# Kernel optimization log

Hardware: AMD Instinct MI355X
Metric: run time of the kernel (lower is better)

Reference implementation:

```python
import jax, jax.numpy as jnp
import numpy as np

BN_EPS = 1e-5


def setup_inputs() -> dict:
    key = jax.random.key(0)
    ks = jax.random.split(key, 12)
    N, E, H, INV = 100000, 500000, 128, 16
    DIN = 2 * H + INV  # 272
    x_send = jax.random.normal(ks[0], (N, H), dtype=jnp.float32)
    x_rec = jax.random.normal(ks[1], (N, H), dtype=jnp.float32)
    index = jax.random.randint(ks[2], (2, E), 0, N, dtype=jnp.int64)
    edge_attr = jax.random.normal(ks[3], (E, INV), dtype=jnp.float32)
    # message_mlp = BatchNorm1d(272) -> Linear(272,128) -> SiLU  (eval-mode BN)
    bn_gamma = jax.random.normal(ks[4], (DIN,), dtype=jnp.float32) * 0.1 + 1.0
    bn_beta = jax.random.normal(ks[5], (DIN,), dtype=jnp.float32) * 0.1
    bn_mean = jax.random.normal(ks[6], (DIN,), dtype=jnp.float32) * 0.1
    bn_var = jax.random.uniform(ks[7], (DIN,), dtype=jnp.float32) + 0.5
    W1 = jax.random.normal(ks[8], (DIN, H), dtype=jnp.float32) / np.sqrt(DIN)
    b1 = jnp.zeros((H,), dtype=jnp.float32)
    # edge_inf_mlp = Linear(128,1) -> Sigmoid
    W2 = jax.random.normal(ks[9], (H, 1), dtype=jnp.float32) / np.sqrt(H)
    b2 = jnp.zeros((1,), dtype=jnp.float32)
    return {"x_send": x_send, "x_rec": x_rec, "index": index, "edge_attr": edge_attr,
            "bn_gamma": bn_gamma, "bn_beta": bn_beta, "bn_mean": bn_mean, "bn_var": bn_var,
            "W1": W1, "b1": b1, "W2": W2, "b2": b2}


def reference(x_send, x_rec, index, edge_attr, bn_gamma, bn_beta, bn_mean, bn_var, W1, b1, W2, b2):
    idx_send, idx_rec = index[0], index[1]
    # gather + concat -> [E, 2H + INV]
    state = jnp.concatenate((x_send[idx_send], x_rec[idx_rec], edge_attr), axis=1)
    # eval-mode BatchNorm1d
    state = (state - bn_mean) * (bn_gamma * jax.lax.rsqrt(bn_var + BN_EPS)) + bn_beta
    # Linear + SiLU
    messages = jax.nn.silu(state @ W1 + b1)  # [E, H]
    # edge gating: Linear(H,1) + Sigmoid
    edge_weights = jax.nn.sigmoid(messages @ W2 + b2)  # [E, 1]
    # scatter_add aggregation over receiving nodes
    return jax.ops.segment_sum(messages * edge_weights, idx_rec, num_segments=x_rec.shape[0])
```

## Files before the change

kernel.cpp:

```cpp
#include <hip/hip_runtime.h>
#include <hip/hip_bf16.h>
#include <hip/hip_fp16.h>
#include <math.h>

#define HDIM 128
#define INVD 16
#define DIN 272
#define NKT 9

typedef __attribute__((ext_vector_type(4))) float f32x4;
typedef __attribute__((ext_vector_type(8))) short bf16x8;
typedef __attribute__((ext_vector_type(2))) __fp16 fp16x2;

__device__ inline short f2bf(float f) {
    union { float f; unsigned u; } v; v.f = f;
    unsigned r = v.u + 0x7FFFu + ((v.u >> 16) & 1u);
    return (short)(r >> 16);
}

template<bool WS>
__global__ __launch_bounds__(256, 2) void etnn_kernel(
    const float* __restrict__ x_send,
    const float* __restrict__ x_rec,
    const int*   __restrict__ index,
    const float* __restrict__ edge_attr,
    const float* __restrict__ bn_gamma,
    const float* __restrict__ bn_beta,
    const float* __restrict__ bn_mean,
    const float* __restrict__ bn_var,
    const float* __restrict__ W1,
    const float* __restrict__ b1,
    const float* __restrict__ W2,
    const float* __restrict__ b2,
    float* __restrict__ out,
    __half* __restrict__ ws,
    int E, int nIter)
{
    __shared__ short btab[NKT * 8 * 64 * 8];
    __shared__ float scl[DIN];
    __shared__ float shf[DIN];
    __shared__ float bias2[2][HDIM];
    __shared__ float biasT[HDIM];

    const int tid = threadIdx.x;
    const int l  = tid & 63;
    const int lr = l & 15;
    const int lg = l >> 4;

    for (int c = tid; c < DIN; c += 256) {
        float sc = bn_gamma[c] * rsqrtf(bn_var[c] + 1e-5f);
        scl[c] = sc;
        shf[c] = bn_beta[c] - bn_mean[c] * sc;
    }
    __syncthreads();

    for (int f = tid; f < NKT * 8 * 64; f += 256) {
        const int kk  = f >> 9;
        const int cb  = (f >> 6) & 7;
        const int ln  = f & 63;
        const int k0  = kk * 32 + (ln >> 4) * 8;
        const int col = cb * 16 + (ln & 15);
        bf16x8 bv;
        #pragma unroll
        for (int j = 0; j < 8; ++j) {
            const int k = k0 + j;
            float v = (k < DIN) ? scl[k] * W1[k * HDIM + col] : 0.f;
            bv[j] = f2bf(v);
        }
        *(bf16x8*)&btab[f * 8] = bv;
    }
    {
        const int col  = tid & 127;
        const int half = tid >> 7;
        float s = 0.f;
        for (int k = half * 136; k < half * 136 + 136; ++k)
            s += shf[k] * W1[k * HDIM + col];
        bias2[half][col] = s;
    }
    __syncthreads();
    if (tid < HDIM) biasT[tid] = b1[tid] + bias2[0][tid] + bias2[1][tid];
    __syncthreads();

    float biasv[8], w2v[8];
    #pragma unroll
    for (int cb = 0; cb < 8; ++cb) {
        biasv[cb] = biasT[cb * 16 + lr];
        w2v[cb]   = W2[cb * 16 + lr];
    }
    const float b2v = b2[0];
    const bool evn = !(lr & 1);

    const int gw = blockIdx.x * 4 + (tid >> 6);
    const int NW = gridDim.x * 4;

    for (int it = gw; it < nIter; it += NW) {
        const int e0 = it * 16;
        const int e  = e0 + lr;
        const int ec = (e < E) ? e : E - 1;
        const int is = index[ec];
        const int ir = index[E + ec];

        const f32x4* ps = (const f32x4*)(x_send + (size_t)is * HDIM);
        const f32x4* pr = (const f32x4*)(x_rec  + (size_t)ir * HDIM);
        f32x4 Ls[8], Lr[8], La[2];
        #pragma unroll
        for (int kk = 0; kk < 4; ++kk) {
            Ls[kk * 2]     = ps[kk * 8 + lg * 2];
            Ls[kk * 2 + 1] = ps[kk * 8 + lg * 2 + 1];
            Lr[kk * 2]     = pr[kk * 8 + lg * 2];
            Lr[kk * 2 + 1] = pr[kk * 8 + lg * 2 + 1];
        }
        if (lg < 2) {
            const f32x4* pa = (const f32x4*)(edge_attr + (size_t)ec * INVD + lg * 8);
            La[0] = pa[0]; La[1] = pa[1];
        } else {
            La[0] = (f32x4){0.f, 0.f, 0.f, 0.f};
            La[1] = (f32x4){0.f, 0.f, 0.f, 0.f};
        }

        f32x4 acc[8];
        #pragma unroll
        for (int cb = 0; cb < 8; ++cb) acc[cb] = (f32x4){0.f, 0.f, 0.f, 0.f};

        #pragma unroll
        for (int kk = 0; kk < NKT; ++kk) {
            f32x4 lo = (kk < 4) ? Ls[kk * 2]     : (kk < 8) ? Lr[(kk - 4) * 2]     : La[0];
            f32x4 hi = (kk < 4) ? Ls[kk * 2 + 1] : (kk < 8) ? Lr[(kk - 4) * 2 + 1] : La[1];
            bf16x8 a;
            a[0] = f2bf(lo[0]); a[1] = f2bf(lo[1]); a[2] = f2bf(lo[2]); a[3] = f2bf(lo[3]);
            a[4] = f2bf(hi[0]); a[5] = f2bf(hi[1]); a[6] = f2bf(hi[2]); a[7] = f2bf(hi[3]);
            #pragma unroll
            for (int cb = 0; cb < 8; ++cb) {
                bf16x8 b = *(const bf16x8*)&btab[((kk * 8 + cb) * 64 + l) * 8];
                acc[cb] = __builtin_amdgcn_mfma_f32_16x16x32_bf16(a, b, acc[cb], 0, 0, 0);
            }
        }

        float p[4] = {0.f, 0.f, 0.f, 0.f};
        #pragma unroll
        for (int cb = 0; cb < 8; ++cb) {
            #pragma unroll
            for (int q = 0; q < 4; ++q) {
                float z = acc[cb][q] + biasv[cb];
                float m = z / (1.f + __expf(-z));
                acc[cb][q] = m;
                p[q] += m * w2v[cb];
            }
        }
        #pragma unroll
        for (int q = 0; q < 4; ++q) {
            p[q] += __shfl_xor(p[q], 1, 64);
            p[q] += __shfl_xor(p[q], 2, 64);
            p[q] += __shfl_xor(p[q], 4, 64);
            p[q] += __shfl_xor(p[q], 8, 64);
        }

        #pragma unroll
        for (int q = 0; q < 4; ++q) {
            const int row = lg * 4 + q;
            if (e0 + row < E) {
                const int irq = __shfl(ir, row, 64);
                const float g = 1.f / (1.f + __expf(-(p[q] + b2v)));
                if constexpr (WS) {
                    float m[8];
                    #pragma unroll
                    for (int cb = 0; cb < 8; ++cb) m[cb] = acc[cb][q] * g;
                    #pragma unroll
                    for (int c = 0; c < 4; ++c) {
                        float x0 = __shfl_xor(m[2 * c],     1, 64);
                        float x1 = __shfl_xor(m[2 * c + 1], 1, 64);
                        float va = evn ? m[2 * c] : x1;
                        float vb = evn ? x0       : m[2 * c + 1];
                        union { fp16x2 h; unsigned u; } pk;
                        pk.h = __builtin_amdgcn_cvt_pkrtz(va, vb);
                        const int col0 = evn ? (32 * c + lr) : (32 * c + 15 + lr);
                        unsigned long long a =
                            (unsigned long long)(ws + (size_t)irq * HDIM + col0);
                        asm volatile("global_atomic_pk_add_f16 %0, %1, off"
                                     :: "v"(a), "v"(pk.u) : "memory");
                    }
                } else {
                    float* orow = out + (size_t)irq * HDIM + lr;
                    #pragma unroll
                    for (int cb = 0; cb < 8; ++cb)
                        atomicAdd(orow + cb * 16, acc[cb][q] * g);
                }
            }
        }
    }
}

__global__ __launch_bounds__(256) void cvt_kernel(const __half* __restrict__ ws,
                                                  float* __restrict__ out, int n) {
    int i = (blockIdx.x * 256 + threadIdx.x) * 4;
    if (i < n) {
        const __half2* p = (const __half2*)(ws + i);
        float2 a = __half22float2(p[0]);
        float2 b = __half22float2(p[1]);
        f32x4 v = {a.x, a.y, b.x, b.y};
        *(f32x4*)(out + i) = v;
    }
}

extern "C" void kernel_launch(void* const* d_in, const int* in_sizes, int n_in,
                              void* d_out, int out_size, void* d_ws, size_t ws_size,
                              hipStream_t stream) {
    const float* x_send    = (const float*)d_in[0];
    const float* x_rec     = (const float*)d_in[1];
    const int*   index     = (const int*)d_in[2];
    const float* edge_attr = (const float*)d_in[3];
    const float* bn_gamma  = (const float*)d_in[4];
    const float* bn_beta   = (const float*)d_in[5];
    const float* bn_mean   = (const float*)d_in[6];
    const float* bn_var    = (const float*)d_in[7];
    const float* W1        = (const float*)d_in[8];
    const float* b1        = (const float*)d_in[9];
    const float* W2        = (const float*)d_in[10];
    const float* b2        = (const float*)d_in[11];
    float* out = (float*)d_out;

    const int E = in_sizes[3] / INVD;
    const int N = in_sizes[0] / HDIM;
    const int nIter = (E + 15) / 16;
    const int grid = 512;

    const size_t need = (size_t)N * HDIM * sizeof(__half);
    if (ws_size >= need) {
        __half* ws = (__half*)d_ws;
        hipMemsetAsync(ws, 0, need, stream);
        etnn_kernel<true><<<grid, 256, 0, stream>>>(x_send, x_rec, index, edge_attr,
                                                    bn_gamma, bn_beta, bn_mean, bn_var,
                                                    W1, b1, W2, b2, out, ws, E, nIter);
        const int n = N * HDIM;
        cvt_kernel<<<(n / 4 + 255) / 256, 256, 0, stream>>>(ws, out, n);
    } else {
        hipMemsetAsync(d_out, 0, (size_t)out_size * sizeof(float), stream);
        etnn_kernel<false><<<grid, 256, 0, stream>>>(x_send, x_rec, index, edge_attr,
                                                     bn_gamma, bn_beta, bn_mean, bn_var,
                                                     W1, b1, W2, b2, out, nullptr, E, nIter);
    }
}
```

Baseline: 193.7 us.

## Sort edges by receiver via counting sort and merge same-node atomics

Adds histogram, single-block scan and fill kernels that build a receiver-sorted edge permutation in the workspace. The main kernel then processes edges in that order and accumulates consecutive messages for the same receiver in registers, issuing fp16 atomics only when the node changes. The aim is fewer scattered atomic operations and better locality for x_rec gathers. In exchange it adds three extra launches, a serial-ish single-block scan over 100k nodes, an extra indirection load, and lanes in a 4-row group rarely share a receiver (average degree about 5), so the merging gains may be small.

```diff
diff --git a/kernel.cpp b/kernel.cpp
--- a/kernel.cpp
+++ b/kernel.cpp
@@ -18,7 +18,42 @@
     return (short)(r >> 16);
 }
 
-template<bool WS>
+__global__ void hist_kernel(const int* __restrict__ index, int* __restrict__ cnt, int E) {
+    int e = blockIdx.x * blockDim.x + threadIdx.x;
+    if (e < E) atomicAdd(&cnt[index[E + e]], 1);
+}
+
+__global__ __launch_bounds__(1024) void scan_kernel(const int* __restrict__ cnt,
+                                                    int* __restrict__ cur, int N) {
+    __shared__ int psum[1024];
+    const int t = threadIdx.x;
+    const int C = (N + 1023) >> 10;
+    const int a0 = t * C;
+    const int a1 = (a0 + C < N) ? a0 + C : N;
+    int s = 0;
+    for (int i = a0; i < a1; ++i) s += cnt[i];
+    psum[t] = s;
+    __syncthreads();
+    for (int d = 1; d < 1024; d <<= 1) {
+        int v = (t >= d) ? psum[t - d] : 0;
+        __syncthreads();
+        psum[t] += v;
+        __syncthreads();
+    }
+    int run = (t > 0) ? psum[t - 1] : 0;
+    for (int i = a0; i < a1; ++i) {
+        cur[i] = run;
+        run += cnt[i];
+    }
+}
+
+__global__ void fill_kernel(const int* __restrict__ index, int* __restrict__ cur,
+                            int* __restrict__ eid, int E) {
+    int e = blockIdx.x * blockDim.x + threadIdx.x;
+    if (e < E) { int p = atomicAdd(&cur[index[E + e]], 1); eid[p] = e; }
+}
+
+template<int MODE>
 __global__ __launch_bounds__(256, 2) void etnn_kernel(
     const float* __restrict__ x_send,
     const float* __restrict__ x_rec,
@@ -32,6 +67,7 @@
     const float* __restrict__ b1,
     const float* __restrict__ W2,
     const float* __restrict__ b2,
+    const int*   __restrict__ eid,
     float* __restrict__ out,
     __half* __restrict__ ws,
     int E, int nIter)
@@ -95,8 +131,9 @@
 
     for (int it = gw; it < nIter; it += NW) {
         const int e0 = it * 16;
-        const int e  = e0 + lr;
-        const int ec = (e < E) ? e : E - 1;
+        const int pos = e0 + lr;
+        const int pc  = (pos < E) ? pos : E - 1;
+        const int ec  = (MODE == 2) ? eid[pc] : pc;
         const int is = index[ec];
         const int ir = index[E + ec];
 
@@ -155,35 +192,74 @@
             p[q] += __shfl_xor(p[q], 8, 64);
         }
 
-        #pragma unroll
-        for (int q = 0; q < 4; ++q) {
-            const int row = lg * 4 + q;
-            if (e0 + row < E) {
-                const int irq = __shfl(ir, row, 64);
-                const float g = 1.f / (1.f + __expf(-(p[q] + b2v)));
-                if constexpr (WS) {
-                    float m[8];
-                    #pragma unroll
-                    for (int cb = 0; cb < 8; ++cb) m[cb] = acc[cb][q] * g;
-                    #pragma unroll
-                    for (int c = 0; c < 4; ++c) {
-                        float x0 = __shfl_xor(m[2 * c],     1, 64);
-                        float x1 = __shfl_xor(m[2 * c + 1], 1, 64);
-                        float va = evn ? m[2 * c] : x1;
-                        float vb = evn ? x0       : m[2 * c + 1];
-                        union { fp16x2 h; unsigned u; } pk;
-                        pk.h = __builtin_amdgcn_cvt_pkrtz(va, vb);
-                        const int col0 = evn ? (32 * c + lr) : (32 * c + 15 + lr);
-                        unsigned long long a =
-                            (unsigned long long)(ws + (size_t)irq * HDIM + col0);
-                        asm volatile("global_atomic_pk_add_f16 %0, %1, off"
-                                     :: "v"(a), "v"(pk.u) : "memory");
+        if constexpr (MODE == 2) {
+            float mm[8];
+            int cur = -1;
+            auto flushf = [&](int node) {
+                #pragma unroll
+                for (int c = 0; c < 4; ++c) {
+                    float x0 = __shfl_xor(mm[2 * c],     1, 64);
+                    float x1 = __shfl_xor(mm[2 * c + 1], 1, 64);
+                    float va = evn ? mm[2 * c] : x1;
+                    float vb = evn ? x0        : mm[2 * c + 1];
+                    union { fp16x2 h; unsigned u; } pk;
+                    pk.h = __builtin_amdgcn_cvt_pkrtz(va, vb);
+                    const int col0 = evn ? (32 * c + lr) : (32 * c + 15 + lr);
+                    unsigned long long a =
+                        (unsigned long long)(ws + (size_t)node * HDIM + col0);
+                    asm volatile("global_atomic_pk_add_f16 %0, %1, off"
+                                 :: "v"(a), "v"(pk.u) : "memory");
+                }
+            };
+            #pragma unroll
+            for (int q = 0; q < 4; ++q) {
+                const int row = lg * 4 + q;
+                if (e0 + row < E) {
+                    const int nq = __shfl(ir, row, 64);
+                    const float g = 1.f / (1.f + __expf(-(p[q] + b2v)));
+                    if (nq != cur) {
+                        if (cur >= 0) flushf(cur);
+                        cur = nq;
+                        #pragma unroll
+                        for (int cb = 0; cb < 8; ++cb) mm[cb] = acc[cb][q] * g;
+                    } else {
+                        #pragma unroll
+                        for (int cb = 0; cb < 8; ++cb) mm[cb] += acc[cb][q] * g;
                     }
-                } else {
-                    float* orow = out + (size_t)irq * HDIM + lr;
-                    #pragma unroll
-                    for (int cb = 0; cb < 8; ++cb)
-                        atomicAdd(orow + cb * 16, acc[cb][q] * g);
+                }
+            }
+            if (cur >= 0) flushf(cur);
+        } else {
+            #pragma unroll
+            for (int q = 0; q < 4; ++q) {
+                const int row = lg * 4 + q;
+                if (e0 + row < E) {
+                    const int irq = __shfl(ir, row, 64);
+                    const float g = 1.f / (1.f + __expf(-(p[q] + b2v)));
+                    if constexpr (MODE == 1) {
+                        float m[8];
+                        #pragma unroll
+                        for (int cb = 0; cb < 8; ++cb) m[cb] = acc[cb][q] * g;
+                        #pragma unroll
+                        for (int c = 0; c < 4; ++c) {
+                            float x0 = __shfl_xor(m[2 * c],     1, 64);
+                            float x1 = __shfl_xor(m[2 * c + 1], 1, 64);
+                            float va = evn ? m[2 * c] : x1;
+                            float vb = evn ? x0       : m[2 * c + 1];
+                            union { fp16x2 h; unsigned u; } pk;
+                            pk.h = __builtin_amdgcn_cvt_pkrtz(va, vb);
+                            const int col0 = evn ? (32 * c + lr) : (32 * c + 15 + lr);
+                            unsigned long long a =
+                                (unsigned long long)(ws + (size_t)irq * HDIM + col0);
+                            asm volatile("global_atomic_pk_add_f16 %0, %1, off"
+                                         :: "v"(a), "v"(pk.u) : "memory");
+                        }
+                    } else {
+                        float* orow = out + (size_t)irq * HDIM + lr;
+                        #pragma unroll
+                        for (int cb = 0; cb < 8; ++cb)
+                            atomicAdd(orow + cb * 16, acc[cb][q] * g);
+                    }
                 }
             }
         }
@@ -224,19 +300,37 @@
     const int nIter = (E + 15) / 16;
     const int grid = 512;
 
-    const size_t need = (size_t)N * HDIM * sizeof(__half);
-    if (ws_size >= need) {
+    const size_t accBytes = (size_t)N * HDIM * sizeof(__half);
+    const size_t accAl    = (accBytes + 255) & ~(size_t)255;
+    const size_t csrBytes = ((size_t)2 * N + (size_t)E) * sizeof(int);
+
+    if (ws_size >= accAl + csrBytes) {
         __half* ws = (__half*)d_ws;
-        hipMemsetAsync(ws, 0, need, stream);
-        etnn_kernel<true><<<grid, 256, 0, stream>>>(x_send, x_rec, index, edge_attr,
-                                                    bn_gamma, bn_beta, bn_mean, bn_var,
-                                                    W1, b1, W2, b2, out, ws, E, nIter);
+        int* cnt = (int*)((char*)d_ws + accAl);
+        int* cur = cnt + N;
+        int* eid = cur + N;
+        hipMemsetAsync(ws, 0, accBytes, stream);
+        hipMemsetAsync(cnt, 0, (size_t)N * sizeof(int), stream);
+        hist_kernel<<<(E + 255) / 256, 256, 0, stream>>>(index, cnt, E);
+        scan_kernel<<<1, 1024, 0, stream>>>(cnt, cur, N);
+        fill_kernel<<<(E + 255) / 256, 256, 0, stream>>>(index, cur, eid, E);
+        etnn_kernel<2><<<grid, 256, 0, stream>>>(x_send, x_rec, index, edge_attr,
+                                                 bn_gamma, bn_beta, bn_mean, bn_var,
+                                                 W1, b1, W2, b2, eid, out, ws, E, nIter);
+        const int n = N * HDIM;
+        cvt_kernel<<<(n / 4 + 255) / 256, 256, 0, stream>>>(ws, out, n);
+    } else if (ws_size >= accBytes) {
+        __half* ws = (__half*)d_ws;
+        hipMemsetAsync(ws, 0, accBytes, stream);
+        etnn_kernel<1><<<grid, 256, 0, stream>>>(x_send, x_rec, index, edge_attr,
+                                                 bn_gamma, bn_beta, bn_mean, bn_var,
+                                                 W1, b1, W2, b2, nullptr, out, ws, E, nIter);
         const int n = N * HDIM;
         cvt_kernel<<<(n / 4 + 255) / 256, 256, 0, stream>>>(ws, out, n);
     } else {
         hipMemsetAsync(d_out, 0, (size_t)out_size * sizeof(float), stream);
-        etnn_kernel<false><<<grid, 256, 0, stream>>>(x_send, x_rec, index, edge_attr,
-                                                     bn_gamma, bn_beta, bn_mean, bn_var,
-                                                     W1, b1, W2, b2, out, nullptr, E, nIter);
-    }
-}
+        etnn_kernel<0><<<grid, 256, 0, stream>>>(x_send, x_rec, index, edge_attr,
+                                                 bn_gamma, bn_beta, bn_mean, bn_var,
+                                                 W1, b1, W2, b2, nullptr, out, nullptr, E, nIter);
+    }
+}
```

New measurement: 380.6 us. 1.97x slower.

## Process two edge tiles per iteration and use packed bf16 conversion

Applied to the files above, without the earlier changes.

Each wave now loads indices and issues the row gathers for two 16-edge tiles before computing either, so more memory loads are in flight to hide gather latency. The manual round-to-nearest bf16 conversion is replaced by the hardware v_cvt_pk_bf16_f32 instruction, which cuts ALU work. Holding two sets of gathered rows in registers roughly doubles register pressure, which under launch_bounds(256,2) risks spilling or lower occupancy.

```diff
diff --git a/kernel.cpp b/kernel.cpp
--- a/kernel.cpp
+++ b/kernel.cpp
@@ -18,7 +18,13 @@
     return (short)(r >> 16);
 }
 
-template<bool WS>
+__device__ inline unsigned cvt_pk_bf16(float a, float b) {
+    unsigned r;
+    asm("v_cvt_pk_bf16_f32 %0, %1, %2" : "=v"(r) : "v"(a), "v"(b));
+    return r;
+}
+
+template<int MODE>
 __global__ __launch_bounds__(256, 2) void etnn_kernel(
     const float* __restrict__ x_send,
     const float* __restrict__ x_rec,
@@ -90,19 +96,10 @@
     const float b2v = b2[0];
     const bool evn = !(lr & 1);
 
-    const int gw = blockIdx.x * 4 + (tid >> 6);
-    const int NW = gridDim.x * 4;
-
-    for (int it = gw; it < nIter; it += NW) {
-        const int e0 = it * 16;
-        const int e  = e0 + lr;
-        const int ec = (e < E) ? e : E - 1;
-        const int is = index[ec];
-        const int ir = index[E + ec];
-
+    auto issueGather = [&](int pc, int is, int ir,
+                           f32x4* Ls, f32x4* Lr, f32x4* La) {
         const f32x4* ps = (const f32x4*)(x_send + (size_t)is * HDIM);
         const f32x4* pr = (const f32x4*)(x_rec  + (size_t)ir * HDIM);
-        f32x4 Ls[8], Lr[8], La[2];
         #pragma unroll
         for (int kk = 0; kk < 4; ++kk) {
             Ls[kk * 2]     = ps[kk * 8 + lg * 2];
@@ -111,13 +108,16 @@
             Lr[kk * 2 + 1] = pr[kk * 8 + lg * 2 + 1];
         }
         if (lg < 2) {
-            const f32x4* pa = (const f32x4*)(edge_attr + (size_t)ec * INVD + lg * 8);
+            const f32x4* pa = (const f32x4*)(edge_attr + (size_t)pc * INVD + lg * 8);
             La[0] = pa[0]; La[1] = pa[1];
         } else {
             La[0] = (f32x4){0.f, 0.f, 0.f, 0.f};
             La[1] = (f32x4){0.f, 0.f, 0.f, 0.f};
         }
-
+    };
+
+    auto computeTile = [&](int e0, int ir,
+                           f32x4* Ls, f32x4* Lr, f32x4* La) {
         f32x4 acc[8];
         #pragma unroll
         for (int cb = 0; cb < 8; ++cb) acc[cb] = (f32x4){0.f, 0.f, 0.f, 0.f};
@@ -126,13 +126,15 @@
         for (int kk = 0; kk < NKT; ++kk) {
             f32x4 lo = (kk < 4) ? Ls[kk * 2]     : (kk < 8) ? Lr[(kk - 4) * 2]     : La[0];
             f32x4 hi = (kk < 4) ? Ls[kk * 2 + 1] : (kk < 8) ? Lr[(kk - 4) * 2 + 1] : La[1];
-            bf16x8 a;
-            a[0] = f2bf(lo[0]); a[1] = f2bf(lo[1]); a[2] = f2bf(lo[2]); a[3] = f2bf(lo[3]);
-            a[4] = f2bf(hi[0]); a[5] = f2bf(hi[1]); a[6] = f2bf(hi[2]); a[7] = f2bf(hi[3]);
+            union { bf16x8 v; unsigned u[4]; } a;
+            a.u[0] = cvt_pk_bf16(lo[0], lo[1]);
+            a.u[1] = cvt_pk_bf16(lo[2], lo[3]);
+            a.u[2] = cvt_pk_bf16(hi[0], hi[1]);
+            a.u[3] = cvt_pk_bf16(hi[2], hi[3]);
             #pragma unroll
             for (int cb = 0; cb < 8; ++cb) {
                 bf16x8 b = *(const bf16x8*)&btab[((kk * 8 + cb) * 64 + l) * 8];
-                acc[cb] = __builtin_amdgcn_mfma_f32_16x16x32_bf16(a, b, acc[cb], 0, 0, 0);
+                acc[cb] = __builtin_amdgcn_mfma_f32_16x16x32_bf16(a.v, b, acc[cb], 0, 0, 0);
             }
         }
 
@@ -161,7 +163,7 @@
             if (e0 + row < E) {
                 const int irq = __shfl(ir, row, 64);
                 const float g = 1.f / (1.f + __expf(-(p[q] + b2v)));
-                if constexpr (WS) {
+                if constexpr (MODE == 1) {
                     float m[8];
                     #pragma unroll
                     for (int cb = 0; cb < 8; ++cb) m[cb] = acc[cb][q] * g;
@@ -187,6 +189,35 @@
                 }
             }
         }
+    };
+
+    const int gw = blockIdx.x * 4 + (tid >> 6);
+    const int NW = gridDim.x * 4;
+
+    for (int it = gw; it < nIter; it += 2 * NW) {
+        const int itB  = it + NW;
+        const bool hasB = itB < nIter;
+
+        const int posA = it * 16 + lr;
+        const int pcA  = (posA < E) ? posA : E - 1;
+        const int isA  = index[pcA];
+        const int irA  = index[E + pcA];
+
+        int pcB = 0, isB = 0, irB = 0;
+        if (hasB) {
+            const int posB = itB * 16 + lr;
+            pcB = (posB < E) ? posB : E - 1;
+            isB = index[pcB];
+            irB = index[E + pcB];
+        }
+
+        f32x4 LsA[8], LrA[8], LaA[2];
+        f32x4 LsB[8], LrB[8], LaB[2];
+        issueGather(pcA, isA, irA, LsA, LrA, LaA);
+        if (hasB) issueGather(pcB, isB, irB, LsB, LrB, LaB);
+
+        computeTile(it * 16, irA, LsA, LrA, LaA);
+        if (hasB) computeTile(itB * 16, irB, LsB, LrB, LaB);
     }
 }
 
@@ -224,19 +255,19 @@
     const int nIter = (E + 15) / 16;
     const int grid = 512;
 
-    const size_t need = (size_t)N * HDIM * sizeof(__half);
-    if (ws_size >= need) {
+    const size_t accBytes = (size_t)N * HDIM * sizeof(__half);
+    if (ws_size >= accBytes) {
         __half* ws = (__half*)d_ws;
-        hipMemsetAsync(ws, 0, need, stream);
-        etnn_kernel<true><<<grid, 256, 0, stream>>>(x_send, x_rec, index, edge_attr,
-                                                    bn_gamma, bn_beta, bn_mean, bn_var,
-                                                    W1, b1, W2, b2, out, ws, E, nIter);
+        hipMemsetAsync(ws, 0, accBytes, stream);
+        etnn_kernel<1><<<grid, 256, 0, stream>>>(x_send, x_rec, index, edge_attr,
+                                                 bn_gamma, bn_beta, bn_mean, bn_var,
+                                                 W1, b1, W2, b2, out, ws, E, nIter);
         const int n = N * HDIM;
         cvt_kernel<<<(n / 4 + 255) / 256, 256, 0, stream>>>(ws, out, n);
     } else {
         hipMemsetAsync(d_out, 0, (size_t)out_size * sizeof(float), stream);
-        etnn_kernel<false><<<grid, 256, 0, stream>>>(x_send, x_rec, index, edge_attr,
-                                                     bn_gamma, bn_beta, bn_mean, bn_var,
-                                                     W1, b1, W2, b2, out, nullptr, E, nIter);
-    }
-}
+        etnn_kernel<0><<<grid, 256, 0, stream>>>(x_send, x_rec, index, edge_attr,
+                                                 bn_gamma, bn_beta, bn_mean, bn_var,
+                                                 W1, b1, W2, b2, out, nullptr, E, nIter);
+    }
+}
```

Result: slower. 221.3 us (+14.3%).
